# Optimization experiments

Measured on AMD Instinct MI355X. Metric: run time of the kernel, lower is better.

The kernel has to match this reference:

```python
import jax, jax.numpy as jnp
import numpy as np

N = 50000
E = 800000
IN_DIM = 10
EMB = 32
HID = 128
LAYERS = 3
BN_EPS = 1e-5


def setup_inputs() -> dict:
    key = jax.random.key(0)
    ks = jax.random.split(key, 16)
    inp = {}
    inp["x"] = jax.random.normal(ks[0], (N, IN_DIM), dtype=jnp.float32)
    inp["edge_index"] = jax.random.randint(ks[1], (2, E), 0, N, dtype=jnp.int64)
    inp["edge_weight"] = jax.random.uniform(ks[2], (E,), dtype=jnp.float32)
    # learned parameters
    inp["emb_table"] = jax.random.normal(ks[3], (N, EMB), dtype=jnp.float32) * 0.02
    inp["ft_W"] = jax.random.normal(ks[4], (EMB, IN_DIM), dtype=jnp.float32) * 0.05
    inp["ft_b"] = jnp.zeros((EMB,), dtype=jnp.float32)
    inp["comb_W"] = jax.random.normal(ks[5], (HID, 2 * EMB), dtype=jnp.float32) * 0.05
    inp["comb_b"] = jnp.zeros((HID,), dtype=jnp.float32)
    inp["conv_W"] = jax.random.normal(ks[6], (LAYERS, HID, HID), dtype=jnp.float32) * 0.05
    inp["conv_b"] = jnp.zeros((LAYERS, HID), dtype=jnp.float32)
    inp["bn_gamma"] = jnp.ones((HID,), dtype=jnp.float32)
    inp["bn_beta"] = jnp.zeros((HID,), dtype=jnp.float32)
    inp["bn_mean"] = jnp.zeros((HID,), dtype=jnp.float32)
    inp["bn_var"] = jnp.ones((HID,), dtype=jnp.float32)
    inp["lin_W"] = jax.random.normal(ks[7], (1, HID), dtype=jnp.float32) * 0.05
    inp["lin_b"] = jnp.zeros((1,), dtype=jnp.float32)
    return inp


def gcn_conv(h, row, col, ew, W, b):
    # PyG GCNConv: x' = D^{-1/2} (A + I) D^{-1/2} x W + b
    n = h.shape[0]
    loop = jnp.arange(n, dtype=row.dtype)
    r = jnp.concatenate([row, loop])          # source nodes
    c = jnp.concatenate([col, loop])          # target nodes
    w = jnp.concatenate([ew, jnp.ones((n,), dtype=ew.dtype)])
    deg = jax.ops.segment_sum(w, c, num_segments=n)
    dinv = jnp.where(deg > 0, jax.lax.rsqrt(deg), 0.0)
    norm = dinv[r] * w * dinv[c]               # [E+N]
    xt = h @ W.T                                # [N, HID]
    msg = xt[r] * norm[:, None]                 # gather + scale
    out = jax.ops.segment_sum(msg, c, num_segments=n)
    return out + b


def reference(x, edge_index, edge_weight, emb_table, ft_W, ft_b, comb_W, comb_b,
              conv_W, conv_b, bn_gamma, bn_beta, bn_mean, bn_var, lin_W, lin_b):
    x = jnp.nan_to_num(x, nan=0.0)
    node_emb = emb_table                        # embedding(arange(N)) == full table
    feat_emb = x @ ft_W.T + ft_b
    combined = jnp.concatenate([node_emb, feat_emb], axis=1)
    h = jax.nn.relu(combined @ comb_W.T + comb_b)
    # dropout disabled (eval mode)
    row, col = edge_index[0], edge_index[1]
    inv_std = jax.lax.rsqrt(bn_var + BN_EPS)
    for i in range(LAYERS):
        h_new = gcn_conv(h, row, col, edge_weight, conv_W[i], conv_b[i])
        h_new = jax.nn.relu(h_new)
        h_new = (h_new - bn_mean) * inv_std * bn_gamma + bn_beta  # BN eval mode
        h = h_new + h                            # residual (shapes always match)
    out = h @ lin_W.T + lin_b
    return jnp.clip(out, -10.0, 10.0)
```

## Files before the change

kernel.cpp:

```cpp
#include <hip/hip_runtime.h>
#include <hip/hip_fp16.h>
#include <math.h>

#define NN 50000
#define EE 800000
#define INDIM 10
#define EMB 32
#define HID 128
#define NLAYERS 3
#define BN_EPS 1e-5f
#define CAP 64

typedef _Float16 h2v __attribute__((ext_vector_type(2)));
__device__ __forceinline__ float fdot2(__half2 a, __half2 b, float c) {
    return __builtin_amdgcn_fdot2(*(h2v*)&a, *(h2v*)&b, c, false);
}

__device__ __forceinline__ int clampN(int v) {
    return v < 0 ? 0 : (v >= NN ? NN - 1 : v);
}

__device__ __forceinline__ void accum8(float acc[8], float4 v, float w) {
    const __half2* hh = (const __half2*)&v;
    #pragma unroll
    for (int k = 0; k < 4; ++k) {
        float2 f = __half22float2(hh[k]);
        acc[2 * k]     = fmaf(f.x, w, acc[2 * k]);
        acc[2 * k + 1] = fmaf(f.y, w, acc[2 * k + 1]);
    }
}


__global__ void k_init(int* __restrict__ cursor) {
    int i = blockIdx.x * blockDim.x + threadIdx.x;
    if (i < NN) cursor[i] = 0;
}

__global__ void k_fill(const int* __restrict__ ei,
                       const float* __restrict__ ew,
                       int* __restrict__ cursor, unsigned* __restrict__ csr) {
    int e = blockIdx.x * blockDim.x + threadIdx.x;
    if (e < EE) {
        int r = clampN(ei[e]);
        int c = clampN(ei[EE + e]);
        int pos = atomicAdd(&cursor[c], 1);
        if (pos >= CAP) pos = CAP - 1;
        unsigned short hw = __half_as_ushort(__float2half(ew[e]));
        unsigned v = (unsigned)(unsigned short)r | ((unsigned)hw << 16);
        __builtin_nontemporal_store(v, &csr[(size_t)c * CAP + pos]);
    }
}

__global__ __launch_bounds__(256) void k_deg(const unsigned* __restrict__ csr,
                                             const int* __restrict__ cnt,
                                             float* __restrict__ dinv) {
    int n = blockIdx.x * 4 + (threadIdx.x >> 6);
    int l = threadIdx.x & 63;
    if (n >= NN) return;
    int m = cnt[n]; if (m > CAP) m = CAP;
    const unsigned* seg = &csr[(size_t)n * CAP];
    float s = 0.f;
    for (int i = l; i < m; i += 64)
        s += __half2float(__ushort_as_half((unsigned short)(seg[i] >> 16)));
    #pragma unroll
    for (int o = 32; o; o >>= 1) s += __shfl_xor(s, o, 64);
    if (l == 0) dinv[n] = rsqrtf(1.0f + s);
}

__global__ void k_wprep(const float* __restrict__ convW,
                        const float* __restrict__ combW,
                        __half2* __restrict__ Wtp, float* __restrict__ Wct) {
    int idx = blockIdx.x * blockDim.x + threadIdx.x;
    const int NWT = NLAYERS * 64 * HID;
    if (idx < NWT) {
        int L = idx / (64 * HID);
        int rem = idx - L * 64 * HID;
        int kk = rem >> 7, c = rem & 127;
        const float* Wl = convW + L * HID * HID + c * HID;
        Wtp[idx] = __floats2half2_rn(Wl[2 * kk], Wl[2 * kk + 1]);
    } else {
        int j = idx - NWT;
        if (j < HID * 2 * EMB) {
            int k = j >> 7, c = j & 127;
            Wct[j] = combW[c * (2 * EMB) + k];
        }
    }
}


__global__ __launch_bounds__(256) void k_init_h(
        const float* __restrict__ x, const float* __restrict__ emb,
        const float* __restrict__ ftW, const float* __restrict__ ftb,
        const float* __restrict__ Wct, const float* __restrict__ combb,
        float* __restrict__ h) {
    __shared__ float csh[64 * 68];
    __shared__ float xsh[64 * INDIM];
    int t = threadIdx.x;
    int n0 = blockIdx.x * 64;

    for (int s = t; s < 64 * INDIM; s += 256) {
        int j = s / INDIM, q = s - j * INDIM;
        float xv = (n0 + j < NN) ? x[(n0 + j) * INDIM + q] : 0.f;
        unsigned bits = __float_as_uint(xv) & 0x7fffffffu;
        if (bits > 0x7f800000u) xv = 0.f;
        xsh[s] = xv;
    }
    #pragma unroll
    for (int i = 0; i < 8; ++i) {
        int s = i * 256 + t;
        int j = s >> 5, k = s & 31;
        csh[j * 68 + k] = (n0 + j < NN) ? emb[(n0 + j) * EMB + k] : 0.f;
    }
    __syncthreads();
    #pragma unroll
    for (int i = 0; i < 8; ++i) {
        int s = i * 256 + t;
        int j = s >> 5, kk = s & 31;
        float acc = ftb[kk];
        #pragma unroll
        for (int q = 0; q < INDIM; ++q)
            acc = fmaf(ftW[kk * INDIM + q], xsh[j * INDIM + q], acc);
        csh[j * 68 + 32 + kk] = acc;
    }
    __syncthreads();

    int ty = t >> 4, tx = t & 15;
    float acc[4][8];
    #pragma unroll
    for (int i = 0; i < 4; ++i)
        #pragma unroll
        for (int j = 0; j < 8; ++j) acc[i][j] = 0.f;

    for (int k0 = 0; k0 < 64; k0 += 4) {
        float wf[4][8];
        #pragma unroll
        for (int kk = 0; kk < 4; ++kk) {
            float4 a = *(const float4*)&Wct[(k0 + kk) * HID + tx * 8];
            float4 b = *(const float4*)&Wct[(k0 + kk) * HID + tx * 8 + 4];
            wf[kk][0] = a.x; wf[kk][1] = a.y; wf[kk][2] = a.z; wf[kk][3] = a.w;
            wf[kk][4] = b.x; wf[kk][5] = b.y; wf[kk][6] = b.z; wf[kk][7] = b.w;
        }
        float hf[4][4];
        #pragma unroll
        for (int i = 0; i < 4; ++i) {
            float4 hv = *(const float4*)&csh[(ty * 4 + i) * 68 + k0];
            hf[i][0] = hv.x; hf[i][1] = hv.y; hf[i][2] = hv.z; hf[i][3] = hv.w;
        }
        #pragma unroll
        for (int i = 0; i < 4; ++i)
            #pragma unroll
            for (int kk = 0; kk < 4; ++kk)
                #pragma unroll
                for (int j = 0; j < 8; ++j)
                    acc[i][j] = fmaf(hf[i][kk], wf[kk][j], acc[i][j]);
    }
    #pragma unroll
    for (int i = 0; i < 4; ++i) {
        int n = n0 + ty * 4 + i;
        if (n < NN) {
            float b0 = combb[tx * 8],     b1 = combb[tx * 8 + 1];
            float b2 = combb[tx * 8 + 2], b3 = combb[tx * 8 + 3];
            float b4 = combb[tx * 8 + 4], b5 = combb[tx * 8 + 5];
            float b6 = combb[tx * 8 + 6], b7 = combb[tx * 8 + 7];
            *(float4*)&h[(size_t)n * HID + tx * 8] = make_float4(
                fmaxf(acc[i][0] + b0, 0.f), fmaxf(acc[i][1] + b1, 0.f),
                fmaxf(acc[i][2] + b2, 0.f), fmaxf(acc[i][3] + b3, 0.f));
            *(float4*)&h[(size_t)n * HID + tx * 8 + 4] = make_float4(
                fmaxf(acc[i][4] + b4, 0.f), fmaxf(acc[i][5] + b5, 0.f),
                fmaxf(acc[i][6] + b6, 0.f), fmaxf(acc[i][7] + b7, 0.f));
        }
    }
}


#define BM 64
__global__ __launch_bounds__(256) void k_gemm(const float* __restrict__ h,
                                              const __half2* __restrict__ Wtp,
                                              const float* __restrict__ dinv,
                                              __half* __restrict__ xt) {
    __shared__ __half2 hsh[BM * 66];
    int t = threadIdx.x;
    int row0 = blockIdx.x * BM;
    #pragma unroll
    for (int i = 0; i < 8; ++i) {
        int s = i * 256 + t;
        int r = s >> 5;
        int cc = s & 31;
        float4 v = make_float4(0.f, 0.f, 0.f, 0.f);
        int row = row0 + r;
        if (row < NN) v = *(const float4*)&h[row * HID + cc * 4];
        hsh[r * 66 + cc * 2]     = __floats2half2_rn(v.x, v.y);
        hsh[r * 66 + cc * 2 + 1] = __floats2half2_rn(v.z, v.w);
    }
    __syncthreads();
    int ty = t >> 4, tx = t & 15;
    float acc[4][8];
    #pragma unroll
    for (int i = 0; i < 4; ++i)
        #pragma unroll
        for (int j = 0; j < 8; ++j) acc[i][j] = 0.f;

    #pragma unroll 2
    for (int k2 = 0; k2 < 64; ++k2) {
        const __half2* wr = &Wtp[k2 * HID + tx * 8];
        __half2 wf[8];
        *(float4*)&wf[0] = *(const float4*)&wr[0];
        *(float4*)&wf[4] = *(const float4*)&wr[4];
        __half2 hf[4];
        #pragma unroll
        for (int i = 0; i < 4; ++i) hf[i] = hsh[(ty * 4 + i) * 66 + k2];
        #pragma unroll
        for (int i = 0; i < 4; ++i)
            #pragma unroll
            for (int j = 0; j < 8; ++j)
                acc[i][j] = fdot2(hf[i], wf[j], acc[i][j]);
    }
    #pragma unroll
    for (int i = 0; i < 4; ++i) {
        int row = row0 + ty * 4 + i;
        if (row < NN) {
            float dv = dinv[row];
            __half2 p0 = __floats2half2_rn(acc[i][0] * dv, acc[i][1] * dv);
            __half2 p1 = __floats2half2_rn(acc[i][2] * dv, acc[i][3] * dv);
            __half2 p2 = __floats2half2_rn(acc[i][4] * dv, acc[i][5] * dv);
            __half2 p3 = __floats2half2_rn(acc[i][6] * dv, acc[i][7] * dv);
            uint4 u = make_uint4(*(unsigned*)&p0, *(unsigned*)&p1,
                                 *(unsigned*)&p2, *(unsigned*)&p3);
            *(uint4*)&xt[(size_t)row * HID + tx * 8] = u;
        }
    }
}


__global__ __launch_bounds__(256) void k_aggregate(
        const __half* __restrict__ xt, float* __restrict__ h,
        const int* __restrict__ cnt, const unsigned* __restrict__ csr,
        const float* __restrict__ dinv,
        const float* __restrict__ bias, const float* __restrict__ gamma,
        const float* __restrict__ beta, const float* __restrict__ mean,
        const float* __restrict__ var,
        const float* __restrict__ linW, const float* __restrict__ linb,
        float* __restrict__ out, int last) {
    int g = threadIdx.x >> 4, q = threadIdx.x & 15;
    int n = blockIdx.x * 16 + g;
    if (n >= NN) return;
    const float4* xt4 = (const float4*)xt;
    const unsigned* seg = &csr[(size_t)n * CAP];
    int m = cnt[n]; if (m > CAP) m = CAP;
    float acc[8];
    #pragma unroll
    for (int j = 0; j < 8; ++j) acc[j] = 0.f;
    int i = 0;
    for (; i + 3 < m; i += 4) {
        unsigned p0 = seg[i],     p1 = seg[i + 1];
        unsigned p2 = seg[i + 2], p3 = seg[i + 3];
        float4 r0 = xt4[(size_t)(p0 & 0xffffu) * 16 + q];
        float4 r1 = xt4[(size_t)(p1 & 0xffffu) * 16 + q];
        float4 r2 = xt4[(size_t)(p2 & 0xffffu) * 16 + q];
        float4 r3 = xt4[(size_t)(p3 & 0xffffu) * 16 + q];
        float w0 = __half2float(__ushort_as_half((unsigned short)(p0 >> 16)));
        float w1 = __half2float(__ushort_as_half((unsigned short)(p1 >> 16)));
        float w2 = __half2float(__ushort_as_half((unsigned short)(p2 >> 16)));
        float w3 = __half2float(__ushort_as_half((unsigned short)(p3 >> 16)));
        accum8(acc, r0, w0);
        accum8(acc, r1, w1);
        accum8(acc, r2, w2);
        accum8(acc, r3, w3);
    }
    for (; i < m; ++i) {
        unsigned p = seg[i];
        float4 r = xt4[(size_t)(p & 0xffffu) * 16 + q];
        float w = __half2float(__ushort_as_half((unsigned short)(p >> 16)));
        accum8(acc, r, w);
    }
    accum8(acc, xt4[(size_t)n * 16 + q], 1.0f);
    float dn = dinv[n];

    int c0 = q * 8;
    float hres[8];
    *(float4*)&hres[0] = *(const float4*)&h[(size_t)n * HID + c0];
    *(float4*)&hres[4] = *(const float4*)&h[(size_t)n * HID + c0 + 4];
    float outv[8];
    #pragma unroll
    for (int j = 0; j < 8; ++j) {
        float v = fmaxf(acc[j] * dn + bias[c0 + j], 0.f);
        v = (v - mean[c0 + j]) * rsqrtf(var[c0 + j] + BN_EPS) * gamma[c0 + j]
            + beta[c0 + j];
        outv[j] = v + hres[j];
    }
    if (!last) {
        *(float4*)&h[(size_t)n * HID + c0]     = *(float4*)&outv[0];
        *(float4*)&h[(size_t)n * HID + c0 + 4] = *(float4*)&outv[4];
    } else {
        float s = 0.f;
        #pragma unroll
        for (int j = 0; j < 8; ++j) s = fmaf(outv[j], linW[c0 + j], s);
        #pragma unroll
        for (int o = 8; o; o >>= 1) s += __shfl_xor(s, o, 64);
        if (q == 0) {
            float o = s + linb[0];
            out[n] = fminf(fmaxf(o, -10.f), 10.f);
        }
    }
}


extern "C" void kernel_launch(void* const* d_in, const int* in_sizes, int n_in,
                              void* d_out, int out_size, void* d_ws, size_t ws_size,
                              hipStream_t stream) {
    const float* x     = (const float*)d_in[0];
    const int*   ei    = (const int*)d_in[1];
    const float* ew    = (const float*)d_in[2];
    const float* emb   = (const float*)d_in[3];
    const float* ftW   = (const float*)d_in[4];
    const float* ftb   = (const float*)d_in[5];
    const float* combW = (const float*)d_in[6];
    const float* combb = (const float*)d_in[7];
    const float* convW = (const float*)d_in[8];
    const float* convb = (const float*)d_in[9];
    const float* gamma = (const float*)d_in[10];
    const float* beta  = (const float*)d_in[11];
    const float* mean  = (const float*)d_in[12];
    const float* var   = (const float*)d_in[13];
    const float* linW  = (const float*)d_in[14];
    const float* linb  = (const float*)d_in[15];
    float* out = (float*)d_out;

    char* ws = (char*)d_ws;
    size_t off = 0;
    auto alloc = [&](size_t bytes) {
        void* p = ws + off;
        off = (off + bytes + 255) & ~(size_t)255;
        return p;
    };
    float*    h    = (float*)alloc((size_t)NN * HID * 4);
    __half*   xt   = (__half*)alloc((size_t)NN * HID * 2);
    float*    dinv = (float*)alloc((size_t)NN * 4);
    int*      cnt  = (int*)alloc((size_t)NN * 4);
    unsigned* csr  = (unsigned*)alloc((size_t)NN * CAP * 4);
    __half2*  Wtp  = (__half2*)alloc((size_t)NLAYERS * 64 * HID * 4);
    float*    Wct  = (float*)alloc((size_t)HID * 2 * EMB * 4);

    const int NBK = (NN + 255) / 256;
    const int EB = (EE + 255) / 256;
    const int NODE4 = (NN + 3) / 4;
    const int AGB = (NN + 15) / 16;
    const int IHB = (NN + 63) / 64;
    const int WPB = (NLAYERS * 64 * HID + HID * 2 * EMB + 255) / 256;

    k_init<<<NBK, 256, 0, stream>>>(cnt);
    k_fill<<<EB, 256, 0, stream>>>(ei, ew, cnt, csr);
    k_deg<<<NODE4, 256, 0, stream>>>(csr, cnt, dinv);
    k_wprep<<<WPB, 256, 0, stream>>>(convW, combW, Wtp, Wct);
    k_init_h<<<IHB, 256, 0, stream>>>(x, emb, ftW, ftb, Wct, combb, h);
    for (int L = 0; L < NLAYERS; ++L) {
        k_gemm<<<(NN + BM - 1) / BM, 256, 0, stream>>>(h, Wtp + (size_t)L * 64 * HID, dinv, xt);
        k_aggregate<<<AGB, 256, 0, stream>>>(xt, h, cnt, csr, dinv,
                                             convb + L * HID, gamma, beta, mean, var,
                                             linW, linb, out, L == NLAYERS - 1);
    }
}
```

Before: 303.9 us.

## Fuse init and weight prep kernels, use fp16 dot2 in input projection, unroll gather by 8

Merges the cursor-zeroing and weight-prep kernels into one launch, dropping a kernel launch. It converts the combine weights and the concatenated embedding/feature tile to packed half2, so the input projection GEMM uses fdot2 and half the shared memory. The aggregation gather loop is unrolled from 4 to 8 to keep more independent loads in flight. The cost is fp16 rounding in the first layer and higher register pressure in the aggregation kernel.

```diff
diff --git a/kernel.cpp b/kernel.cpp
--- a/kernel.cpp
+++ b/kernel.cpp
@@ -31,9 +31,27 @@
 }
 
 
-__global__ void k_init(int* __restrict__ cursor) {
-    int i = blockIdx.x * blockDim.x + threadIdx.x;
-    if (i < NN) cursor[i] = 0;
+#define NWT (NLAYERS * 64 * HID)
+#define NWC (32 * HID)
+
+__global__ void k_prep(const float* __restrict__ convW,
+                       const float* __restrict__ combW,
+                       __half2* __restrict__ Wtp, __half2* __restrict__ Wctp,
+                       int* __restrict__ cursor) {
+    int idx = blockIdx.x * blockDim.x + threadIdx.x;
+    if (idx < NN) cursor[idx] = 0;
+    if (idx < NWT) {
+        int L = idx / (64 * HID);
+        int rem = idx - L * 64 * HID;
+        int kk = rem >> 7, c = rem & 127;
+        const float* Wl = convW + L * HID * HID + c * HID;
+        Wtp[idx] = __floats2half2_rn(Wl[2 * kk], Wl[2 * kk + 1]);
+    } else if (idx - NWT < NWC) {
+        int j = idx - NWT;
+        int kk = j >> 7, c = j & 127;
+        const float* Wc = combW + c * (2 * EMB);
+        Wctp[j] = __floats2half2_rn(Wc[2 * kk], Wc[2 * kk + 1]);
+    }
 }
 
 __global__ void k_fill(const int* __restrict__ ei,
@@ -67,33 +85,13 @@
     if (l == 0) dinv[n] = rsqrtf(1.0f + s);
 }
 
-__global__ void k_wprep(const float* __restrict__ convW,
-                        const float* __restrict__ combW,
-                        __half2* __restrict__ Wtp, float* __restrict__ Wct) {
-    int idx = blockIdx.x * blockDim.x + threadIdx.x;
-    const int NWT = NLAYERS * 64 * HID;
-    if (idx < NWT) {
-        int L = idx / (64 * HID);
-        int rem = idx - L * 64 * HID;
-        int kk = rem >> 7, c = rem & 127;
-        const float* Wl = convW + L * HID * HID + c * HID;
-        Wtp[idx] = __floats2half2_rn(Wl[2 * kk], Wl[2 * kk + 1]);
-    } else {
-        int j = idx - NWT;
-        if (j < HID * 2 * EMB) {
-            int k = j >> 7, c = j & 127;
-            Wct[j] = combW[c * (2 * EMB) + k];
-        }
-    }
-}
-
 
 __global__ __launch_bounds__(256) void k_init_h(
         const float* __restrict__ x, const float* __restrict__ emb,
         const float* __restrict__ ftW, const float* __restrict__ ftb,
-        const float* __restrict__ Wct, const float* __restrict__ combb,
+        const __half2* __restrict__ Wctp, const float* __restrict__ combb,
         float* __restrict__ h) {
-    __shared__ float csh[64 * 68];
+    __shared__ __half2 csh2[64 * 34];
     __shared__ float xsh[64 * INDIM];
     int t = threadIdx.x;
     int n0 = blockIdx.x * 64;
@@ -105,22 +103,29 @@
         if (bits > 0x7f800000u) xv = 0.f;
         xsh[s] = xv;
     }
-    #pragma unroll
-    for (int i = 0; i < 8; ++i) {
-        int s = i * 256 + t;
-        int j = s >> 5, k = s & 31;
-        csh[j * 68 + k] = (n0 + j < NN) ? emb[(n0 + j) * EMB + k] : 0.f;
-    }
     __syncthreads();
     #pragma unroll
     for (int i = 0; i < 8; ++i) {
         int s = i * 256 + t;
         int j = s >> 5, kk = s & 31;
-        float acc = ftb[kk];
-        #pragma unroll
-        for (int q = 0; q < INDIM; ++q)
-            acc = fmaf(ftW[kk * INDIM + q], xsh[j * INDIM + q], acc);
-        csh[j * 68 + 32 + kk] = acc;
+        int n = n0 + j;
+        __half2 v;
+        if (kk < 16) {
+            float2 e2 = (n < NN) ? *(const float2*)&emb[(size_t)n * EMB + 2 * kk]
+                                 : make_float2(0.f, 0.f);
+            v = __floats2half2_rn(e2.x, e2.y);
+        } else {
+            int f0 = 2 * (kk - 16);
+            float a0 = ftb[f0], a1 = ftb[f0 + 1];
+            #pragma unroll
+            for (int q = 0; q < INDIM; ++q) {
+                float xv = xsh[j * INDIM + q];
+                a0 = fmaf(ftW[f0 * INDIM + q], xv, a0);
+                a1 = fmaf(ftW[(f0 + 1) * INDIM + q], xv, a1);
+            }
+            v = __floats2half2_rn(a0, a1);
+        }
+        csh2[j * 34 + kk] = v;
     }
     __syncthreads();
 
@@ -131,43 +136,30 @@
         #pragma unroll
         for (int j = 0; j < 8; ++j) acc[i][j] = 0.f;
 
-    for (int k0 = 0; k0 < 64; k0 += 4) {
-        float wf[4][8];
-        #pragma unroll
-        for (int kk = 0; kk < 4; ++kk) {
-            float4 a = *(const float4*)&Wct[(k0 + kk) * HID + tx * 8];
-            float4 b = *(const float4*)&Wct[(k0 + kk) * HID + tx * 8 + 4];
-            wf[kk][0] = a.x; wf[kk][1] = a.y; wf[kk][2] = a.z; wf[kk][3] = a.w;
-            wf[kk][4] = b.x; wf[kk][5] = b.y; wf[kk][6] = b.z; wf[kk][7] = b.w;
-        }
-        float hf[4][4];
-        #pragma unroll
-        for (int i = 0; i < 4; ++i) {
-            float4 hv = *(const float4*)&csh[(ty * 4 + i) * 68 + k0];
-            hf[i][0] = hv.x; hf[i][1] = hv.y; hf[i][2] = hv.z; hf[i][3] = hv.w;
-        }
+    #pragma unroll 2
+    for (int k2 = 0; k2 < 32; ++k2) {
+        const __half2* wr = &Wctp[k2 * HID + tx * 8];
+        __half2 wf[8];
+        *(float4*)&wf[0] = *(const float4*)&wr[0];
+        *(float4*)&wf[4] = *(const float4*)&wr[4];
+        __half2 hf[4];
+        #pragma unroll
+        for (int i = 0; i < 4; ++i) hf[i] = csh2[(ty * 4 + i) * 34 + k2];
         #pragma unroll
         for (int i = 0; i < 4; ++i)
             #pragma unroll
-            for (int kk = 0; kk < 4; ++kk)
-                #pragma unroll
-                for (int j = 0; j < 8; ++j)
-                    acc[i][j] = fmaf(hf[i][kk], wf[kk][j], acc[i][j]);
+            for (int j = 0; j < 8; ++j)
+                acc[i][j] = fdot2(hf[i], wf[j], acc[i][j]);
     }
     #pragma unroll
     for (int i = 0; i < 4; ++i) {
         int n = n0 + ty * 4 + i;
         if (n < NN) {
-            float b0 = combb[tx * 8],     b1 = combb[tx * 8 + 1];
-            float b2 = combb[tx * 8 + 2], b3 = combb[tx * 8 + 3];
-            float b4 = combb[tx * 8 + 4], b5 = combb[tx * 8 + 5];
-            float b6 = combb[tx * 8 + 6], b7 = combb[tx * 8 + 7];
-            *(float4*)&h[(size_t)n * HID + tx * 8] = make_float4(
-                fmaxf(acc[i][0] + b0, 0.f), fmaxf(acc[i][1] + b1, 0.f),
-                fmaxf(acc[i][2] + b2, 0.f), fmaxf(acc[i][3] + b3, 0.f));
-            *(float4*)&h[(size_t)n * HID + tx * 8 + 4] = make_float4(
-                fmaxf(acc[i][4] + b4, 0.f), fmaxf(acc[i][5] + b5, 0.f),
-                fmaxf(acc[i][6] + b6, 0.f), fmaxf(acc[i][7] + b7, 0.f));
+            #pragma unroll
+            for (int j = 0; j < 8; ++j)
+                acc[i][j] = fmaxf(acc[i][j] + combb[tx * 8 + j], 0.f);
+            *(float4*)&h[(size_t)n * HID + tx * 8]     = *(float4*)&acc[i][0];
+            *(float4*)&h[(size_t)n * HID + tx * 8 + 4] = *(float4*)&acc[i][4];
         }
     }
 }
@@ -251,21 +243,19 @@
     #pragma unroll
     for (int j = 0; j < 8; ++j) acc[j] = 0.f;
     int i = 0;
-    for (; i + 3 < m; i += 4) {
-        unsigned p0 = seg[i],     p1 = seg[i + 1];
-        unsigned p2 = seg[i + 2], p3 = seg[i + 3];
-        float4 r0 = xt4[(size_t)(p0 & 0xffffu) * 16 + q];
-        float4 r1 = xt4[(size_t)(p1 & 0xffffu) * 16 + q];
-        float4 r2 = xt4[(size_t)(p2 & 0xffffu) * 16 + q];
-        float4 r3 = xt4[(size_t)(p3 & 0xffffu) * 16 + q];
-        float w0 = __half2float(__ushort_as_half((unsigned short)(p0 >> 16)));
-        float w1 = __half2float(__ushort_as_half((unsigned short)(p1 >> 16)));
-        float w2 = __half2float(__ushort_as_half((unsigned short)(p2 >> 16)));
-        float w3 = __half2float(__ushort_as_half((unsigned short)(p3 >> 16)));
-        accum8(acc, r0, w0);
-        accum8(acc, r1, w1);
-        accum8(acc, r2, w2);
-        accum8(acc, r3, w3);
+    for (; i + 7 < m; i += 8) {
+        unsigned p_[8];
+        #pragma unroll
+        for (int u = 0; u < 8; ++u) p_[u] = seg[i + u];
+        float4 r_[8];
+        #pragma unroll
+        for (int u = 0; u < 8; ++u)
+            r_[u] = xt4[(size_t)(p_[u] & 0xffffu) * 16 + q];
+        #pragma unroll
+        for (int u = 0; u < 8; ++u) {
+            float w = __half2float(__ushort_as_half((unsigned short)(p_[u] >> 16)));
+            accum8(acc, r_[u], w);
+        }
     }
     for (; i < m; ++i) {
         unsigned p = seg[i];
@@ -338,21 +328,19 @@
     float*    dinv = (float*)alloc((size_t)NN * 4);
     int*      cnt  = (int*)alloc((size_t)NN * 4);
     unsigned* csr  = (unsigned*)alloc((size_t)NN * CAP * 4);
-    __half2*  Wtp  = (__half2*)alloc((size_t)NLAYERS * 64 * HID * 4);
-    float*    Wct  = (float*)alloc((size_t)HID * 2 * EMB * 4);
+    __half2*  Wtp  = (__half2*)alloc((size_t)NWT * 4);
+    __half2*  Wctp = (__half2*)alloc((size_t)NWC * 4);
 
     const int NBK = (NN + 255) / 256;
     const int EB = (EE + 255) / 256;
     const int NODE4 = (NN + 3) / 4;
     const int AGB = (NN + 15) / 16;
     const int IHB = (NN + 63) / 64;
-    const int WPB = (NLAYERS * 64 * HID + HID * 2 * EMB + 255) / 256;
-
-    k_init<<<NBK, 256, 0, stream>>>(cnt);
+
+    k_prep<<<NBK, 256, 0, stream>>>(convW, combW, Wtp, Wctp, cnt);
     k_fill<<<EB, 256, 0, stream>>>(ei, ew, cnt, csr);
     k_deg<<<NODE4, 256, 0, stream>>>(csr, cnt, dinv);
-    k_wprep<<<WPB, 256, 0, stream>>>(convW, combW, Wtp, Wct);
-    k_init_h<<<IHB, 256, 0, stream>>>(x, emb, ftW, ftb, Wct, combb, h);
+    k_init_h<<<IHB, 256, 0, stream>>>(x, emb, ftW, ftb, Wctp, combb, h);
     for (int L = 0; L < NLAYERS; ++L) {
         k_gemm<<<(NN + BM - 1) / BM, 256, 0, stream>>>(h, Wtp + (size_t)L * 64 * HID, dinv, xt);
         k_aggregate<<<AGB, 256, 0, stream>>>(xt, h, cnt, csr, dinv,
```

Result: no change. 301.2 us (-0.9%).
